# Kernel optimization log

Measured on AMD Instinct MI355X. Metric: run time of the kernel, lower is better.

Reference implementation:

```python
import jax, jax.numpy as jnp
import numpy as np

B, L, D, H, HD = 2, 8192, 1024, 16, 64
MINI = 64
NC = L // MINI
TTT_BASE_LR = 1.0
NUM_CHUNKS = 4
TEXT_LEN = 64
INIT_OFFSET = 2048


def setup_inputs() -> dict:
    key = jax.random.key(0)
    ks = jax.random.split(key, 16)
    hidden_states = jax.random.normal(ks[0], (B, L, D), dtype=jnp.float32)
    # llama-style rope table as (cos, sin) pairs: [L, HD//2, 2]
    inv_freq = 1.0 / (10000.0 ** (np.arange(0, HD, 2, dtype=np.float32) / HD))
    t = np.arange(L, dtype=np.float32)
    ang = np.outer(t, inv_freq)  # [L, HD//2]
    freqs_cis = jnp.asarray(np.stack([np.cos(ang), np.sin(ang)], axis=-1))
    std = 0.02
    inp = {"hidden_states": hidden_states, "freqs_cis": freqs_cis}
    names = ["wq", "wk", "wv", "wu"]
    for i, n in enumerate(names):
        inp[n + "_w"] = jax.random.normal(ks[1 + i], (D, D), dtype=jnp.float32) * std  # [in, out]
        inp[n + "_b"] = jnp.zeros((D,), dtype=jnp.float32)
    inp["ttt_norm_weight"] = jnp.ones((H, HD), dtype=jnp.float32)
    inp["ttt_norm_bias"] = jnp.zeros((H, HD), dtype=jnp.float32)
    inp["lr_weight"] = jax.random.normal(ks[6], (H, 1, D), dtype=jnp.float32) * std
    inp["lr_bias"] = jnp.zeros((H, 1), dtype=jnp.float32)
    return inp


def _l2norm(x):
    return x / jnp.maximum(jnp.linalg.norm(x, axis=-1, keepdims=True), 1e-12)


def _rope(x, cos, sin):
    # x: [B, L, H, HD]; cos/sin: [L, HD//2] -> broadcast [1, L, 1, HD//2]
    c = cos[None, :, None, :]
    s = sin[None, :, None, :]
    xr, xi = x[..., 0::2], x[..., 1::2]
    out_r = xr * c - xi * s
    out_i = xr * s + xi * c
    return jnp.stack([out_r, out_i], axis=-1).reshape(x.shape)


def _interleave(x):
    # x: [B, H, NC, C, F]; splice text chunks into video scenes (static offsets)
    b, h, nc, c, f = x.shape
    xf = x.reshape(b, h, nc * c, f)
    stl = TEXT_LEN * NUM_CHUNKS
    x_text = xf[:, :, :stl]
    x_video = xf[:, :, stl:]
    texts = jnp.split(x_text, NUM_CHUNKS, axis=2)
    vio = INIT_OFFSET - TEXT_LEN
    vids = [x_video[:, :, :vio]] + list(jnp.split(x_video[:, :, vio:], NUM_CHUNKS - 1, axis=2))
    pieces = [jnp.concatenate([texts[i], vids[i]], axis=2) for i in range(NUM_CHUNKS)]
    return jnp.concatenate(pieces, axis=2).reshape(b, h, nc, c, f)


def reference(hidden_states, freqs_cis, wq_w, wq_b, wk_w, wk_b, wv_w, wv_b,
              wu_w, wu_b, ttt_norm_weight, ttt_norm_bias, lr_weight, lr_bias):
    X = hidden_states  # [B, L, D]
    XQ = (X @ wq_w + wq_b).reshape(B, L, H, HD)
    XK = (X @ wk_w + wk_b).reshape(B, L, H, HD)
    XV = (X @ wv_w + wv_b).reshape(B, L, H, HD)
    XU = (X @ wu_w + wu_b).reshape(B, L, H, HD)

    XQ, XK, XU = _l2norm(XQ), _l2norm(XK), _l2norm(XU)

    # seq_text_length = 0 in process_input -> rope over the whole sequence
    cos, sin = freqs_cis[..., 0], freqs_cis[..., 1]
    XQ = _rope(XQ, cos, sin)
    XK = _rope(XK, cos, sin)
    XU = _rope(XU, cos, sin)

    # ln reconstruction target (std uses Bessel correction like torch.std)
    diff = XV - XK
    mean = diff.mean(axis=-1, keepdims=True)
    std = jnp.std(diff, axis=-1, keepdims=True, ddof=1)
    norm = (diff - mean) / (std + 1e-8)
    XV = ttt_norm_weight[None, None] * norm + ttt_norm_bias[None, None] + XK

    # reshape to mini-batches: [B, H, NC, C, HD]
    def to_mb(t):
        return t.transpose(0, 2, 1, 3).reshape(B, H, NC, MINI, HD)
    XQ, XK, XV, XU = to_mb(XQ), to_mb(XK), to_mb(XV), to_mb(XU)
    Xmb = X.reshape(B, NC, MINI, D)

    # per-head LR gating
    ttt_lr = jnp.einsum('bnkc,hdc->bhnkd', Xmb, lr_weight) + lr_bias.reshape(1, -1, 1, 1, 1)
    ttt_lr = jax.nn.sigmoid(ttt_lr).transpose(0, 1, 2, 4, 3)  # [B, H, NC, 1, C]
    ttt_lr = TTT_BASE_LR * ttt_lr / HD
    eta = (1.0 / MINI) * jnp.tile(ttt_lr, (1, 1, 1, MINI, 1))  # [B, H, NC, C, C]

    XQ, XK, XV, XU = _interleave(XQ), _interleave(XK), _interleave(XV), _interleave(XU)
    eta = _interleave(eta)

    # HD == MINI == 64 so all five stack cleanly
    return jnp.stack([XQ, XK, XV, XU, eta], axis=0)
```

## Files before the change

kernel.cpp:

```cpp
#include <hip/hip_runtime.h>

typedef unsigned int u32;
typedef unsigned short u16;
typedef short short8v __attribute__((ext_vector_type(8)));
typedef float f32x4 __attribute__((ext_vector_type(4)));

#define ND 1024
#define NH 16
#define OUT_T ((size_t)16777216)

__device__ __forceinline__ u16 f2bf(float f) {
  u32 u = __float_as_uint(f);
  u32 r = u + 0x7fffu + ((u >> 16) & 1u);
  return (u16)(r >> 16);
}

__device__ __forceinline__ short8v pack8(float4 a, float4 b) {
  short8v v;
  v[0] = (short)f2bf(a.x); v[1] = (short)f2bf(a.y);
  v[2] = (short)f2bf(a.z); v[3] = (short)f2bf(a.w);
  v[4] = (short)f2bf(b.x); v[5] = (short)f2bf(b.y);
  v[6] = (short)f2bf(b.z); v[7] = (short)f2bf(b.w);
  return v;
}

__device__ __forceinline__ void gload16(const void* g, void* l) {
  __builtin_amdgcn_global_load_lds((const __attribute__((address_space(1))) void*)g,
                                   (__attribute__((address_space(3))) void*)l, 16, 0, 0);
}

__global__ void k_wt(const float* __restrict__ w0, const float* __restrict__ w1,
                     const float* __restrict__ w2, const float* __restrict__ w3,
                     u16* __restrict__ WT) {
  __shared__ float T[64][65];
  int bid = blockIdx.x;
  int w = bid >> 8;
  int tk = (bid >> 4) & 15, tc = bid & 15;
  const float* W = w == 0 ? w0 : w == 1 ? w1 : w == 2 ? w2 : w3;
  int k0 = tk << 6, c0 = tc << 6;
  int tid = threadIdx.x;
  for (int it = 0; it < 16; ++it) {
    int idx = it * 256 + tid;
    int kk = idx >> 6, cc = idx & 63;
    T[kk][cc] = W[(size_t)(k0 + kk) * ND + c0 + cc];
  }
  __syncthreads();
  for (int it = 0; it < 2; ++it) {
    int ci = it * 256 + tid;
    int cc = ci >> 3, k8 = ci & 7;
    short8v v;
    for (int j = 0; j < 8; ++j) v[j] = (short)f2bf(T[k8 * 8 + j][cc]);
    size_t off = ((((size_t)(w * 16 + tc) * 128) + (tk << 3) + k8) * 64 + cc) * 8;
    *(short8v*)(WT + off) = v;
  }
}

__global__ void k_xbf(const float* __restrict__ X, u16* __restrict__ Xb) {
  size_t i = ((size_t)blockIdx.x * 256 + threadIdx.x) * 8;
  float4 a = *(const float4*)(X + i), b = *(const float4*)(X + i + 4);
  *(short8v*)(Xb + i) = pack8(a, b);
}

__global__ __launch_bounds__(256) void k_lr2(const u16* __restrict__ Xb,
                                             const float* __restrict__ LW,
                                             const float* __restrict__ LB,
                                             float* __restrict__ out) {
  __shared__ __align__(16) char smem[46080];
  u16* LWs = (u16*)smem;
  u16* As = (u16*)(smem + 32768);
  float* El = (float*)(smem + 40960);
  const int tid = threadIdx.x, lane = tid & 63, wid = tid >> 6;
  const int l15 = lane & 15, lg = lane >> 4;
  const int n = blockIdx.x;
  const int tok0 = n << 6;

  {
    int row = tid >> 4;
    int cbase = (tid & 15) << 3;
    const float* src = LW + row * ND + (cbase << 3);
    for (int i = 0; i < 8; ++i) {
      float4 a = *(const float4*)(src + i * 8);
      float4 b = *(const float4*)(src + i * 8 + 4);
      int sc = (cbase + i) ^ (row & 7);
      *(short8v*)(LWs + row * 1024 + (sc << 3)) = pack8(a, b);
    }
  }

  const int arow0 = (wid << 4) + (lane >> 3);
  const u16* asrc = Xb + (size_t)(tok0 + arow0) * ND + ((((lane & 7) ^ arow0) & 7) << 3);
  const u32 aldo = wid << 10;
  const int aoff = ((wid << 4) + l15) << 6;
  const int key = l15 & 7;

  f32x4 acc;
  for (int r = 0; r < 4; ++r) acc[r] = 0.f;
  __syncthreads();

  for (int kt = 0; kt < 16; ++kt) {
    gload16(asrc + (kt << 6), As + aldo);
    gload16(asrc + (kt << 6) + 8 * ND, As + aldo + 512);
    __syncthreads();
    for (int ks = 0; ks < 2; ++ks) {
      int kcl = (ks << 2) + lg;
      int kcg = (kt << 3) + kcl;
      short8v af = *(const short8v*)(As + aoff + ((kcl ^ key) << 3));
      short8v bf = *(const short8v*)(LWs + (l15 << 10) + ((kcg ^ key) << 3));
      acc = __builtin_amdgcn_mfma_f32_16x16x32_bf16(af, bf, acc, 0, 0, 0);
    }
    __syncthreads();
  }

  for (int rr = 0; rr < 4; ++rr) {
    float v = acc[rr] + LB[l15];
    float e = (1.f / (1.f + expf(-v))) * (1.f / 4096.f);
    El[l15 * 72 + (wid << 4) + (lg << 2) + rr] = e;
  }
  __syncthreads();

  const int b = n >> 7, nl = n & 127;
  int q, rc;
  if (nl < 4) { q = nl; rc = 0; }
  else { q = (nl - 4) / 31; rc = nl - 3 - 31 * q; }
  const int pc = q * 32 + rc;
  const int j = tid >> 2, kq = tid & 3;
  size_t base = 4 * OUT_T + (((size_t)(b * NH) << 13) + (pc << 6)) * 64 + (size_t)j * 64;
  for (int h = 0; h < 16; ++h) {
    float* po = out + base + ((size_t)h << 19);
    for (int qq = 0; qq < 4; ++qq) {
      int k0 = (kq + (qq << 2)) << 2;
      const float* ep = El + h * 72 + k0;
      f32x4 t; t[0] = ep[0]; t[1] = ep[1]; t[2] = ep[2]; t[3] = ep[3];
      *(f32x4*)(po + k0) = t;
    }
  }
}

__global__ __launch_bounds__(256, 2) void k_main(
    const u16* __restrict__ Xb, const float* __restrict__ FC,
    const u16* __restrict__ WT,
    const float* __restrict__ qb, const float* __restrict__ kb,
    const float* __restrict__ vb, const float* __restrict__ ub,
    const float* __restrict__ tw, const float* __restrict__ tb,
    float* __restrict__ out) {
  __shared__ __align__(16) char smem[16896];
  float* Cs = (float*)smem;

  const int tid = threadIdx.x;
  const int lane = tid & 63;
  const int w = tid >> 6;
  const int l15 = lane & 15, lg = lane >> 4;
  const int xcd = blockIdx.x & 7;
  const int local = blockIdx.x >> 3;
  const int h = (xcd << 1) | (local >> 7);
  const int s0 = (local & 127) << 7;

  f32x4 acc[8][4];
  for (int i = 0; i < 8; ++i)
    for (int j = 0; j < 4; ++j)
      for (int r = 0; r < 4; ++r) acc[i][j][r] = 0.f;

  const float* bp = (w == 0) ? qb : (w == 1) ? kb : (w == 2) ? vb : ub;
  float biasv[4];
  for (int fn = 0; fn < 4; ++fn) biasv[fn] = bp[h * 64 + fn * 16 + l15];

  const int rS = (w << 5) + (lane >> 2);
  const int chp = lane & 3;
  const u16* asrc = Xb + (size_t)(s0 + rS) * ND + ((chp ^ ((rS >> 1) & 3)) << 3);
  const u32 aldo = w << 10;

  const u16* Bg = WT + (((size_t)(w * 16 + h)) << 16);

  int aoff[8], akey[8];
  for (int f = 0; f < 8; ++f) {
    int ra = (f << 4) + l15;
    aoff[f] = ra << 5; akey[f] = (ra >> 1) & 3;
  }

  gload16(asrc, (u16*)smem + aldo);
  gload16(asrc + 16 * ND, (u16*)smem + aldo + 512);
  short8v bc0, bc1, bc2, bc3, bn0, bn1, bn2, bn3;
  {
    const u16* bb = Bg + ((lg * 64 + l15) << 3);
    bc0 = *(const short8v*)(bb);
    bc1 = *(const short8v*)(bb + 128);
    bc2 = *(const short8v*)(bb + 256);
    bc3 = *(const short8v*)(bb + 384);
  }
  __syncthreads();

  for (int kt = 0; kt < 32; ++kt) {
    const int cur = kt & 1;
    if (kt < 31) {
      const int k0n = (kt + 1) << 5;
      u16* ad = (u16*)smem + ((cur ^ 1) << 12);
      gload16(asrc + k0n, ad + aldo);
      gload16(asrc + k0n + 16 * ND, ad + aldo + 512);
      const u16* bb = Bg + ((((kt + 1) << 2) + lg) << 9) + (l15 << 3);
      bn0 = *(const short8v*)(bb);
      bn1 = *(const short8v*)(bb + 128);
      bn2 = *(const short8v*)(bb + 256);
      bn3 = *(const short8v*)(bb + 384);
    }
    const u16* As = (const u16*)smem + (cur << 12);
    short8v af[8];
#pragma unroll
    for (int f = 0; f < 8; ++f)
      af[f] = *(const short8v*)(As + aoff[f] + ((lg ^ akey[f]) << 3));
    __builtin_amdgcn_s_setprio(1);
#pragma unroll
    for (int fm = 0; fm < 8; ++fm) {
      acc[fm][0] = __builtin_amdgcn_mfma_f32_16x16x32_bf16(af[fm], bc0, acc[fm][0], 0, 0, 0);
      acc[fm][1] = __builtin_amdgcn_mfma_f32_16x16x32_bf16(af[fm], bc1, acc[fm][1], 0, 0, 0);
      acc[fm][2] = __builtin_amdgcn_mfma_f32_16x16x32_bf16(af[fm], bc2, acc[fm][2], 0, 0, 0);
      acc[fm][3] = __builtin_amdgcn_mfma_f32_16x16x32_bf16(af[fm], bc3, acc[fm][3], 0, 0, 0);
    }
    __builtin_amdgcn_s_setprio(0);
    __syncthreads();
    bc0 = bn0; bc1 = bn1; bc2 = bn2; bc3 = bn3;
  }

#pragma unroll
  for (int ph = 0; ph < 8; ++ph) {
    for (int fn = 0; fn < 4; ++fn)
      for (int rr = 0; rr < 4; ++rr) {
        int rl = (lg << 2) + rr;
        int col = (w << 6) + (fn << 4) + l15;
        Cs[rl * 261 + col] = acc[ph][fn][rr] + biasv[fn];
      }
    __syncthreads();
    {
      int tloc = tid >> 4, o = tid & 15;
      int dbase = o << 2;
      int stok = s0 + (ph << 4) + tloc;
      int b = stok >> 13, seq = stok & 8191;
      const float* crow = Cs + tloc * 261;
      f32x4 fc = *(const f32x4*)(FC + ((size_t)seq << 6) + dbase);
      f32x4 vq = *(const f32x4*)(crow + dbase);
      f32x4 vk = *(const f32x4*)(crow + 64 + dbase);
      f32x4 vv = *(const f32x4*)(crow + 128 + dbase);
      f32x4 vu = *(const f32x4*)(crow + 192 + dbase);
      float sq = 0.f, sk = 0.f, su = 0.f;
      for (int j = 0; j < 4; ++j) {
        sq += vq[j] * vq[j]; sk += vk[j] * vk[j]; su += vu[j] * vu[j];
      }
      sq += __shfl_xor(sq, 1); sq += __shfl_xor(sq, 2);
      sq += __shfl_xor(sq, 4); sq += __shfl_xor(sq, 8);
      sk += __shfl_xor(sk, 1); sk += __shfl_xor(sk, 2);
      sk += __shfl_xor(sk, 4); sk += __shfl_xor(sk, 8);
      su += __shfl_xor(su, 1); su += __shfl_xor(su, 2);
      su += __shfl_xor(su, 4); su += __shfl_xor(su, 8);
      float qi = 1.f / fmaxf(sqrtf(sq), 1e-12f);
      float ki = 1.f / fmaxf(sqrtf(sk), 1e-12f);
      float ui = 1.f / fmaxf(sqrtf(su), 1e-12f);
      int p;
      if (seq < 256) p = ((seq >> 6) << 11) + (seq & 63);
      else { int v = seq - 256; int qc = v / 1984; p = (qc << 11) + 64 + (v - qc * 1984); }
      float* po = out + ((((size_t)(b * NH + h) << 13) + p) << 6) + dbase;
      f32x4 kr;
      kr[0] = vk[0] * ki * fc[0] - vk[1] * ki * fc[1];
      kr[1] = vk[0] * ki * fc[1] + vk[1] * ki * fc[0];
      kr[2] = vk[2] * ki * fc[2] - vk[3] * ki * fc[3];
      kr[3] = vk[2] * ki * fc[3] + vk[3] * ki * fc[2];
      *(f32x4*)(po + OUT_T) = kr;
      f32x4 df;
      float sd = 0.f, sdd = 0.f;
      for (int j = 0; j < 4; ++j) {
        df[j] = vv[j] - kr[j];
        sd += df[j]; sdd += df[j] * df[j];
      }
      sd += __shfl_xor(sd, 1); sd += __shfl_xor(sd, 2);
      sd += __shfl_xor(sd, 4); sd += __shfl_xor(sd, 8);
      sdd += __shfl_xor(sdd, 1); sdd += __shfl_xor(sdd, 2);
      sdd += __shfl_xor(sdd, 4); sdd += __shfl_xor(sdd, 8);
      float mean = sd * (1.f / 64.f);
      float var = (sdd - sd * sd * (1.f / 64.f)) * (1.f / 63.f);
      float istd = 1.f / (sqrtf(fmaxf(var, 0.f)) + 1e-8f);
      f32x4 twv = *(const f32x4*)(tw + h * 64 + dbase);
      f32x4 tbv = *(const f32x4*)(tb + h * 64 + dbase);
      f32x4 vo;
      for (int j = 0; j < 4; ++j)
        vo[j] = twv[j] * ((df[j] - mean) * istd) + tbv[j] + kr[j];
      *(f32x4*)(po + 2 * OUT_T) = vo;
      f32x4 qr;
      qr[0] = vq[0] * qi * fc[0] - vq[1] * qi * fc[1];
      qr[1] = vq[0] * qi * fc[1] + vq[1] * qi * fc[0];
      qr[2] = vq[2] * qi * fc[2] - vq[3] * qi * fc[3];
      qr[3] = vq[2] * qi * fc[3] + vq[3] * qi * fc[2];
      *(f32x4*)po = qr;
      qr[0] = vu[0] * ui * fc[0] - vu[1] * ui * fc[1];
      qr[1] = vu[0] * ui * fc[1] + vu[1] * ui * fc[0];
      qr[2] = vu[2] * ui * fc[2] - vu[3] * ui * fc[3];
      qr[3] = vu[2] * ui * fc[3] + vu[3] * ui * fc[2];
      *(f32x4*)(po + 3 * OUT_T) = qr;
    }
    __syncthreads();
  }
}

extern "C" void kernel_launch(void* const* d_in, const int* in_sizes, int n_in,
                              void* d_out, int out_size, void* d_ws, size_t ws_size,
                              hipStream_t stream) {
  const float* X  = (const float*)d_in[0];
  const float* FC = (const float*)d_in[1];
  const float* wq = (const float*)d_in[2];
  const float* qb = (const float*)d_in[3];
  const float* wk = (const float*)d_in[4];
  const float* kb = (const float*)d_in[5];
  const float* wv = (const float*)d_in[6];
  const float* vb = (const float*)d_in[7];
  const float* wu = (const float*)d_in[8];
  const float* ub = (const float*)d_in[9];
  const float* tw = (const float*)d_in[10];
  const float* tb = (const float*)d_in[11];
  const float* lw = (const float*)d_in[12];
  const float* lb = (const float*)d_in[13];
  float* out = (float*)d_out;
  u16* WT = (u16*)d_ws;
  u16* Xb = (u16*)((char*)d_ws + (8u << 20));

  hipLaunchKernelGGL(k_wt, dim3(1024), dim3(256), 0, stream, wq, wk, wv, wu, WT);
  hipLaunchKernelGGL(k_xbf, dim3(8192), dim3(256), 0, stream, X, Xb);
  hipLaunchKernelGGL(k_lr2, dim3(256), dim3(256), 0, stream, Xb, lw, lb, out);
  hipLaunchKernelGGL(k_main, dim3(2048), dim3(256), 0, stream,
                     Xb, FC, WT, qb, kb, vb, ub, tw, tb, out);
}
```

Before: 234.0 us.

## Deepen GEMM A-tile pipeline to four LDS stages with explicit vmcnt waits

The K-loop now keeps A tiles in a four-slot LDS ring with two tiles in flight, and is unrolled by two with ping-pong B register buffers. Each __syncthreads is replaced by a raw s_barrier plus a targeted s_waitcnt vmcnt(6), so the barrier waits only for the oldest stage instead of draining all outstanding loads. The aim is to hide global-load latency behind the MFMAs. In exchange LDS per block roughly doubles to about 33.5 KB, which may limit occupancy, and hand-written waitcnt counts risk races if the compiler reorders the loads.

```diff
diff --git a/kernel.cpp b/kernel.cpp
--- a/kernel.cpp
+++ b/kernel.cpp
@@ -8,6 +8,10 @@
 #define ND 1024
 #define NH 16
 #define OUT_T ((size_t)16777216)
+
+#define SBAR() __builtin_amdgcn_s_barrier()
+#define VMW(n) asm volatile("s_waitcnt vmcnt(" #n ")" ::: "memory")
+#define LGKM0() asm volatile("s_waitcnt lgkmcnt(0)" ::: "memory")
 
 __device__ __forceinline__ u16 f2bf(float f) {
   u32 u = __float_as_uint(f);
@@ -142,7 +146,7 @@
     const float* __restrict__ vb, const float* __restrict__ ub,
     const float* __restrict__ tw, const float* __restrict__ tb,
     float* __restrict__ out) {
-  __shared__ __align__(16) char smem[16896];
+  __shared__ __align__(16) char smem[33536];
   float* Cs = (float*)smem;
 
   const int tid = threadIdx.x;
@@ -168,7 +172,7 @@
   const u16* asrc = Xb + (size_t)(s0 + rS) * ND + ((chp ^ ((rS >> 1) & 3)) << 3);
   const u32 aldo = w << 10;
 
-  const u16* Bg = WT + (((size_t)(w * 16 + h)) << 16);
+  const u16* Bg = WT + (((size_t)(w * 16 + h)) << 16) + (lg << 9) + (l15 << 3);
 
   int aoff[8], akey[8];
   for (int f = 0; f < 8; ++f) {
@@ -176,48 +180,66 @@
     aoff[f] = ra << 5; akey[f] = (ra >> 1) & 3;
   }
 
-  gload16(asrc, (u16*)smem + aldo);
-  gload16(asrc + 16 * ND, (u16*)smem + aldo + 512);
-  short8v bc0, bc1, bc2, bc3, bn0, bn1, bn2, bn3;
-  {
-    const u16* bb = Bg + ((lg * 64 + l15) << 3);
-    bc0 = *(const short8v*)(bb);
-    bc1 = *(const short8v*)(bb + 128);
-    bc2 = *(const short8v*)(bb + 256);
-    bc3 = *(const short8v*)(bb + 384);
-  }
-  __syncthreads();
-
-  for (int kt = 0; kt < 32; ++kt) {
-    const int cur = kt & 1;
-    if (kt < 31) {
-      const int k0n = (kt + 1) << 5;
-      u16* ad = (u16*)smem + ((cur ^ 1) << 12);
-      gload16(asrc + k0n, ad + aldo);
-      gload16(asrc + k0n + 16 * ND, ad + aldo + 512);
-      const u16* bb = Bg + ((((kt + 1) << 2) + lg) << 9) + (l15 << 3);
-      bn0 = *(const short8v*)(bb);
-      bn1 = *(const short8v*)(bb + 128);
-      bn2 = *(const short8v*)(bb + 256);
-      bn3 = *(const short8v*)(bb + 384);
-    }
-    const u16* As = (const u16*)smem + (cur << 12);
-    short8v af[8];
-#pragma unroll
-    for (int f = 0; f < 8; ++f)
-      af[f] = *(const short8v*)(As + aoff[f] + ((lg ^ akey[f]) << 3));
-    __builtin_amdgcn_s_setprio(1);
-#pragma unroll
-    for (int fm = 0; fm < 8; ++fm) {
-      acc[fm][0] = __builtin_amdgcn_mfma_f32_16x16x32_bf16(af[fm], bc0, acc[fm][0], 0, 0, 0);
-      acc[fm][1] = __builtin_amdgcn_mfma_f32_16x16x32_bf16(af[fm], bc1, acc[fm][1], 0, 0, 0);
-      acc[fm][2] = __builtin_amdgcn_mfma_f32_16x16x32_bf16(af[fm], bc2, acc[fm][2], 0, 0, 0);
-      acc[fm][3] = __builtin_amdgcn_mfma_f32_16x16x32_bf16(af[fm], bc3, acc[fm][3], 0, 0, 0);
-    }
-    __builtin_amdgcn_s_setprio(0);
-    __syncthreads();
-    bc0 = bn0; bc1 = bn1; bc2 = bn2; bc3 = bn3;
-  }
+#define STAGE_A(t) do { \
+    u16* ad = (u16*)smem + (((t) & 3) << 12); \
+    gload16(asrc + ((t) << 5), ad + aldo); \
+    gload16(asrc + ((t) << 5) + 16 * ND, ad + aldo + 512); \
+  } while (0)
+
+#define LOAD_B(dst, t) do { \
+    const u16* bb = Bg + ((t) << 11); \
+    dst[0] = *(const short8v*)(bb); \
+    dst[1] = *(const short8v*)(bb + 128); \
+    dst[2] = *(const short8v*)(bb + 256); \
+    dst[3] = *(const short8v*)(bb + 384); \
+  } while (0)
+
+#define READ_A(af, t) do { \
+    const u16* As_ = (const u16*)smem + (((t) & 3) << 12); \
+    _Pragma("unroll") \
+    for (int f = 0; f < 8; ++f) \
+      af[f] = *(const short8v*)(As_ + aoff[f] + ((lg ^ akey[f]) << 3)); \
+  } while (0)
+
+#define MFMA16(af, bv, ofs) do { \
+    __builtin_amdgcn_s_setprio(1); \
+    _Pragma("unroll") \
+    for (int fm = 0; fm < 8; ++fm) { \
+      acc[fm][0] = __builtin_amdgcn_mfma_f32_16x16x32_bf16(af[fm], bv[0], acc[fm][0], 0, 0, 0); \
+      acc[fm][1] = __builtin_amdgcn_mfma_f32_16x16x32_bf16(af[fm], bv[1], acc[fm][1], 0, 0, 0); \
+      acc[fm][2] = __builtin_amdgcn_mfma_f32_16x16x32_bf16(af[fm], bv[2], acc[fm][2], 0, 0, 0); \
+      acc[fm][3] = __builtin_amdgcn_mfma_f32_16x16x32_bf16(af[fm], bv[3], acc[fm][3], 0, 0, 0); \
+    } \
+    __builtin_amdgcn_s_setprio(0); \
+  } while (0)
+
+  STAGE_A(0);
+  STAGE_A(1);
+  short8v b0[4], b1[4];
+  LOAD_B(b0, 0);
+  VMW(4);
+  SBAR();
+
+  short8v af[8];
+  for (int kt2 = 0; kt2 < 16; ++kt2) {
+    const int e = kt2 << 1;
+    READ_A(af, e);
+    if (e < 30) STAGE_A(e + 2);
+    LOAD_B(b1, e + 1);
+    MFMA16(af, b0, e);
+    VMW(6);
+    SBAR();
+    READ_A(af, e + 1);
+    if (e + 1 < 30) STAGE_A(e + 3);
+    if (e + 1 < 31) LOAD_B(b0, e + 2);
+    MFMA16(af, b1, e + 1);
+    if (e + 1 < 31) {
+      VMW(6);
+      SBAR();
+    }
+  }
+  LGKM0();
+  SBAR();
 
 #pragma unroll
   for (int ph = 0; ph < 8; ++ph) {
@@ -227,7 +249,8 @@
         int col = (w << 6) + (fn << 4) + l15;
         Cs[rl * 261 + col] = acc[ph][fn][rr] + biasv[fn];
       }
-    __syncthreads();
+    LGKM0();
+    SBAR();
     {
       int tloc = tid >> 4, o = tid & 15;
       int dbase = o << 2;
@@ -293,7 +316,8 @@
       qr[3] = vu[2] * ui * fc[3] + vu[3] * ui * fc[2];
       *(f32x4*)(po + 3 * OUT_T) = qr;
     }
-    __syncthreads();
+    LGKM0();
+    SBAR();
   }
 }
 
```

Result: slower. 240.0 us (+2.6%).
